# Optimization experiments

Hardware: AMD Instinct MI355X
Metric: run time of the kernel (lower is better)

The kernel has to match this reference:

```python
import jax, jax.numpy as jnp
import numpy as np

DIM = 768
DEPTH = 6
HEADS = 12
DIM_HEAD = 64
INNER = HEADS * DIM_HEAD  # 768
MLP = DIM * 4
B, N = 4, 2048
EPS = 1e-5


def setup_inputs() -> dict:
    key = jax.random.key(0)
    ks = jax.random.split(key, 8)
    s = lambda *sh: 0.02
    inp = {
        "x": jax.random.normal(ks[0], (B, N, DIM), dtype=jnp.float32),
        "ln1_g": jnp.ones((DEPTH, DIM), jnp.float32),
        "ln1_b": jnp.zeros((DEPTH, DIM), jnp.float32),
        "wqkv": jax.random.normal(ks[1], (DEPTH, DIM, 3 * INNER), jnp.float32) * 0.02,
        "wout": jax.random.normal(ks[2], (DEPTH, INNER, DIM), jnp.float32) * 0.02,
        "ln2_g": jnp.ones((DEPTH, DIM), jnp.float32),
        "ln2_b": jnp.zeros((DEPTH, DIM), jnp.float32),
        "w1": jax.random.normal(ks[3], (DEPTH, DIM, MLP), jnp.float32) * 0.02,
        "b1": jnp.zeros((DEPTH, MLP), jnp.float32),
        "w2": jax.random.normal(ks[4], (DEPTH, MLP, DIM), jnp.float32) * 0.02,
        "b2": jnp.zeros((DEPTH, DIM), jnp.float32),
        "fn_g": jnp.ones((DIM,), jnp.float32),
        "fn_b": jnp.zeros((DIM,), jnp.float32),
    }
    return inp


def layer_norm(x, g, b):
    mu = jnp.mean(x, axis=-1, keepdims=True)
    var = jnp.mean(jnp.square(x - mu), axis=-1, keepdims=True)
    return (x - mu) * jax.lax.rsqrt(var + EPS) * g + b


def attention(x, wqkv, wout):
    # x: [b, n, dim]
    qkv = x @ wqkv  # [b, n, 3*inner]
    q, k, v = jnp.split(qkv, 3, axis=-1)
    split_heads = lambda t: t.reshape(t.shape[0], t.shape[1], HEADS, DIM_HEAD).transpose(0, 2, 1, 3)
    q, k, v = split_heads(q), split_heads(k), split_heads(v)  # [b, h, n, d]
    scale = DIM_HEAD ** -0.5
    dots = jnp.einsum("bhnd,bhmd->bhnm", q, k) * scale
    attn = jax.nn.softmax(dots, axis=-1)
    out = jnp.einsum("bhnm,bhmd->bhnd", attn, v)
    out = out.transpose(0, 2, 1, 3).reshape(x.shape[0], x.shape[1], INNER)
    return out @ wout


def feed_forward(x, w1, b1, w2, b2):
    h = jax.nn.gelu(x @ w1 + b1, approximate=False)
    return h @ w2 + b2


def reference(x, ln1_g, ln1_b, wqkv, wout, ln2_g, ln2_b, w1, b1, w2, b2, fn_g, fn_b):
    for i in range(DEPTH):
        x = x + attention(layer_norm(x, ln1_g[i], ln1_b[i]), wqkv[i], wout[i])
        x = x + feed_forward(layer_norm(x, ln2_g[i], ln2_b[i]), w1[i], b1[i], w2[i], b2[i])
    return layer_norm(x, fn_g, fn_b)
```

## Files before the change

kernel.cpp:

```cpp
#include <hip/hip_runtime.h>
#include <hip/hip_bf16.h>

typedef unsigned short ushort_t;
typedef unsigned int uint_t;
typedef __bf16 bf16x8 __attribute__((ext_vector_type(8)));
typedef float floatx4 __attribute__((ext_vector_type(4)));
typedef float floatx16 __attribute__((ext_vector_type(16)));

#define DIM 768
#define DEPTH 6
#define HEADS 12
#define DH 64
#define MLP_DIM 3072
#define BATCH 4
#define SEQ 2048
#define MTOK (BATCH * SEQ)
#define QKV3 (3 * DIM)

__device__ __forceinline__ float bf2f(unsigned u) {
    return __uint_as_float((u & 0xffffu) << 16);
}
__device__ __forceinline__ ushort_t f2bf(float f) {
    unsigned x = __float_as_uint(f);
    return (ushort_t)((x + 0x7FFFu + ((x >> 16) & 1u)) >> 16);
}
__device__ __forceinline__ void load_lds16(const void* g, void* l) {
    __builtin_amdgcn_global_load_lds((const __attribute__((address_space(1))) uint_t*)g,
                                     (__attribute__((address_space(3))) uint_t*)l, 16, 0, 0);
}
__device__ __forceinline__ uint_t cvt_pk_bf16(float lo, float hi) {
    uint_t r;
    asm("v_cvt_pk_bf16_f32 %0, %1, %2" : "=v"(r) : "v"(lo), "v"(hi));
    return r;
}
__device__ __forceinline__ float exp2_raw(float x) {
#if __has_builtin(__builtin_amdgcn_exp2f)
    return __builtin_amdgcn_exp2f(x);
#else
    return exp2f(x);
#endif
}

__global__ __launch_bounds__(256) void transpose_cvt(const float* __restrict__ in,
                                                     ushort_t* __restrict__ out,
                                                     int K, int N) {
    __shared__ float tile[32][33];
    const int d = blockIdx.z;
    in += (size_t)d * K * N;
    out += (size_t)d * K * N;
    const int n0 = blockIdx.x * 32, k0 = blockIdx.y * 32;
    for (int i = threadIdx.y; i < 32; i += 8) {
        tile[i][threadIdx.x] = in[(size_t)(k0 + i) * N + n0 + threadIdx.x];
    }
    __syncthreads();
    for (int i = threadIdx.y; i < 32; i += 8) {
        out[(size_t)(n0 + i) * K + k0 + threadIdx.x] = f2bf(tile[threadIdx.x][i]);
    }
}

template <bool OUTBF>
__global__ __launch_bounds__(256) void layernorm_k(const float* __restrict__ x,
                                                   const float* __restrict__ g,
                                                   const float* __restrict__ bta,
                                                   void* __restrict__ out) {
    const int row = blockIdx.x, t = threadIdx.x;
    const float* xr = x + (size_t)row * DIM;
    float v0 = xr[t], v1 = xr[t + 256], v2 = xr[t + 512];
    float s = v0 + v1 + v2;
    float sq = v0 * v0 + v1 * v1 + v2 * v2;
#pragma unroll
    for (int off = 32; off > 0; off >>= 1) {
        s += __shfl_down(s, off, 64);
        sq += __shfl_down(sq, off, 64);
    }
    __shared__ float ss[4], ssq[4];
    const int w = t >> 6;
    if ((t & 63) == 0) { ss[w] = s; ssq[w] = sq; }
    __syncthreads();
    s = ss[0] + ss[1] + ss[2] + ss[3];
    sq = ssq[0] + ssq[1] + ssq[2] + ssq[3];
    const float mean = s * (1.0f / DIM);
    const float var = sq * (1.0f / DIM) - mean * mean;
    const float rstd = rsqrtf(var + 1e-5f);
    float y0 = (v0 - mean) * rstd * g[t] + bta[t];
    float y1 = (v1 - mean) * rstd * g[t + 256] + bta[t + 256];
    float y2 = (v2 - mean) * rstd * g[t + 512] + bta[t + 512];
    if (OUTBF) {
        ushort_t* o = (ushort_t*)out + (size_t)row * DIM;
        o[t] = f2bf(y0); o[t + 256] = f2bf(y1); o[t + 512] = f2bf(y2);
    } else {
        float* o = (float*)out + (size_t)row * DIM;
        o[t] = y0; o[t + 256] = y1; o[t + 512] = y2;
    }
}

template <bool BIAS, bool GELU, bool RES, bool OUTBF>
__global__ __launch_bounds__(512) void gemm8(const ushort_t* __restrict__ A,
                                             const ushort_t* __restrict__ Bt,
                                             const float* __restrict__ bias,
                                             const float* __restrict__ resid,
                                             void* __restrict__ Cout,
                                             int M, int N, int K) {
    __shared__ ushort_t lds[3 * 24576];
    const int t = threadIdx.x;
    const int lane = t & 63, w = t >> 6;
    const int wm = w >> 2, wn = w & 3;

    const int nwg = gridDim.x * gridDim.y;
    int bid = blockIdx.y * gridDim.x + blockIdx.x;
    bid = (bid & 7) * (nwg >> 3) + (bid >> 3);
    const int bx = bid % gridDim.x, by = bid / gridDim.x;
    const int bm = by * 128, bn = bx * 256;

    floatx4 acc[4][4];
#pragma unroll
    for (int i = 0; i < 4; i++)
#pragma unroll
        for (int j = 0; j < 4; j++) acc[i][j] = (floatx4)0.0f;

    const int srow = t >> 3;
    const int sw = ((t & 7) ^ ((t >> 3) & 7)) * 8;
    const ushort_t* Ab = A + (size_t)(bm + srow) * K + sw;
    const ushort_t* Bb = Bt + (size_t)(bn + srow) * K + sw;

    const int nk = K >> 6;
    auto stage = [&](int kt) {
        ushort_t* ls = lds + (kt % 3) * 24576;
        const int k0 = kt * 64;
        load_lds16(Ab + k0, ls + t * 8);
        load_lds16(Ab + (size_t)64 * K + k0, ls + 4096 + t * 8);
        ushort_t* lb = ls + 8192;
        load_lds16(Bb + k0, lb + t * 8);
        load_lds16(Bb + (size_t)64 * K + k0, lb + 4096 + t * 8);
        load_lds16(Bb + (size_t)128 * K + k0, lb + 8192 + t * 8);
        load_lds16(Bb + (size_t)192 * K + k0, lb + 12288 + t * 8);
    };

    stage(0);
    if (nk > 1) stage(1);

    const int l15 = lane & 15, quad = lane >> 4;
    const int arow = wm * 64 + l15;
    const int brow = wn * 64 + l15;
    const int swz = l15 & 7;

    for (int kt = 0; kt < nk; kt++) {
        if (kt < nk - 1) asm volatile("s_waitcnt vmcnt(6)" ::: "memory");
        else             asm volatile("s_waitcnt vmcnt(0)" ::: "memory");
        __builtin_amdgcn_s_barrier();
        if (kt + 2 < nk) stage(kt + 2);
        const ushort_t* Al = lds + (kt % 3) * 24576;
        const ushort_t* Bl = Al + 8192;
#pragma unroll
        for (int ks = 0; ks < 2; ks++) {
            const int kc = ((ks * 4 + quad) ^ swz) * 8;
            bf16x8 af[4], bf[4];
#pragma unroll
            for (int i = 0; i < 4; i++)
                af[i] = *(const bf16x8*)(Al + (arow + i * 16) * 64 + kc);
#pragma unroll
            for (int j = 0; j < 4; j++)
                bf[j] = *(const bf16x8*)(Bl + (brow + j * 16) * 64 + kc);
#pragma unroll
            for (int i = 0; i < 4; i++)
#pragma unroll
                for (int j = 0; j < 4; j++)
                    acc[i][j] = __builtin_amdgcn_mfma_f32_16x16x32_bf16(af[i], bf[j], acc[i][j], 0, 0, 0);
        }
    }

    const int colq = lane & 15, rq = lane >> 4;
#pragma unroll
    for (int j = 0; j < 4; j++) {
        const int col = bn + wn * 64 + j * 16 + colq;
        const float bv = BIAS ? bias[col] : 0.0f;
#pragma unroll
        for (int i = 0; i < 4; i++) {
#pragma unroll
            for (int r = 0; r < 4; r++) {
                const int row = bm + wm * 64 + i * 16 + rq * 4 + r;
                float v = acc[i][j][r] + bv;
                if (GELU) v = 0.5f * v * (1.0f + erff(v * 0.70710678118654752f));
                const size_t idx = (size_t)row * N + col;
                if (RES) v += resid[idx];
                if (OUTBF) ((ushort_t*)Cout)[idx] = f2bf(v);
                else ((float*)Cout)[idx] = v;
            }
        }
    }
}

#define TSTR 66

__global__ __launch_bounds__(256) void v_transpose(const ushort_t* __restrict__ qkv,
                                                   ushort_t* __restrict__ vt) {
    __shared__ ushort_t tile[64 * TSTR];
    const int t = threadIdx.x;
    const int tk = blockIdx.x, h = blockIdx.y, b = blockIdx.z;
#pragma unroll
    for (int rep = 0; rep < 2; rep++) {
        const int s = t + rep * 256;
        const int row = s >> 3, uo = (s & 7) * 8;
        *(uint4*)(tile + row * TSTR + uo) =
            *(const uint4*)(qkv + (size_t)(b * SEQ + tk * 64 + row) * QKV3 + 2 * DIM + h * DH + uo);
    }
    __syncthreads();
#pragma unroll
    for (int rep = 0; rep < 2; rep++) {
        const int s = t + rep * 256;
        const int d = s >> 3, to = (s & 7) * 8;
        ushort_t tmp[8];
#pragma unroll
        for (int j = 0; j < 8; j++) tmp[j] = tile[(to + j) * TSTR + d];
        *(uint4*)(vt + ((size_t)(b * HEADS + h) * DH + d) * SEQ + tk * 64 + to) = *(uint4*)tmp;
    }
}

#define SC2 0.18033688011112042f

__global__ __launch_bounds__(256, 3) void attn_mfma(const ushort_t* __restrict__ qkv,
                                                    const ushort_t* __restrict__ vt,
                                                    ushort_t* __restrict__ outp) {
    __shared__ ushort_t lds_k[2][64 * 64];
    __shared__ ushort_t lds_vt[2][64 * 64];

    const int t = threadIdx.x;
    const int lane = t & 63, w = t >> 6;
    const int h = blockIdx.y, b = blockIdx.z;
    const int q0 = blockIdx.x * 128 + w * 32;
    const int l31 = lane & 31, hi = lane >> 5;

    bf16x8 qf[4];
#pragma unroll
    for (int dc = 0; dc < 4; dc++) {
        const uint4 raw = *(const uint4*)(qkv + (size_t)(b * SEQ + q0 + l31) * QKV3 +
                                          h * DH + dc * 16 + hi * 8);
        const uint_t rr[4] = {raw.x, raw.y, raw.z, raw.w};
        union { ushort_t u[8]; bf16x8 v; } qq;
#pragma unroll
        for (int e = 0; e < 4; e++) {
            qq.u[2 * e] = f2bf(bf2f(rr[e]) * SC2);
            qq.u[2 * e + 1] = f2bf(bf2f(rr[e] >> 16) * SC2);
        }
        qf[dc] = qq.v;
    }

    union { ushort_t u[8]; bf16x8 v; } onef;
#pragma unroll
    for (int e = 0; e < 8; e++) onef.u[e] = 0x3F80;

    floatx16 o[2];
    o[0] = (floatx16)0.0f; o[1] = (floatx16)0.0f;
    floatx16 osum = (floatx16)0.0f;

    const int srow = w * 16 + (lane >> 3);
    const int sg = ((lane & 7) ^ ((lane >> 3) & 7)) * 8;
    const ushort_t* kgbase = qkv + (size_t)(b * SEQ + srow) * QKV3 + DIM + h * DH + sg;
    const ushort_t* vgbase = vt + ((size_t)(b * HEADS + h) * DH + srow) * SEQ + sg;

    auto stage = [&](int kt) {
        const int bsel = kt & 1;
        ushort_t* ldk = (ushort_t*)lds_k[bsel] + w * 16 * 64;
        ushort_t* ldv = (ushort_t*)lds_vt[bsel] + w * 16 * 64;
        const ushort_t* kg = kgbase + (size_t)kt * 64 * QKV3;
        const ushort_t* vg = vgbase + kt * 64;
        load_lds16(kg, ldk);
        load_lds16(kg + (size_t)8 * QKV3, ldk + 8 * 64);
        load_lds16(vg, ldv);
        load_lds16(vg + (size_t)8 * SEQ, ldv + 8 * 64);
    };

    stage(0);
    for (int kt = 0; kt < SEQ / 64; kt++) {
        __syncthreads();
        stage((kt + 1) & (SEQ / 64 - 1));
        const ushort_t* ldk = lds_k[kt & 1];
        const ushort_t* ldv = lds_vt[kt & 1];

#pragma unroll
        for (int kt2 = 0; kt2 < 2; kt2++) {
            const int krow = kt2 * 32 + l31;
            const int ksw = krow & 7;
            floatx16 s = (floatx16)0.0f;
#pragma unroll
            for (int dc = 0; dc < 4; dc++) {
                const bf16x8 kf = *(const bf16x8*)(ldk + krow * 64 + ((dc * 2 + hi) ^ ksw) * 8);
                s = __builtin_amdgcn_mfma_f32_32x32x16_bf16(kf, qf[dc], s, 0, 0, 0);
            }

            bf16x8 vfr[2][2];
#pragma unroll
            for (int kc = 0; kc < 2; kc++)
#pragma unroll
                for (int dhalf = 0; dhalf < 2; dhalf++) {
                    const int vrow = dhalf * 32 + l31;
                    const int kcg = kt2 * 2 + kc;
                    vfr[kc][dhalf] =
                        *(const bf16x8*)(ldv + vrow * 64 + (((kcg * 2 + hi) ^ (vrow & 7)) * 8));
                }

            float p[16];
#pragma unroll
            for (int r = 0; r < 16; r++) p[r] = exp2_raw(s[r]);

#pragma unroll
            for (int kc = 0; kc < 2; kc++) {
                uint_t da = cvt_pk_bf16(p[kc * 8 + 0], p[kc * 8 + 1]);
                uint_t db = cvt_pk_bf16(p[kc * 8 + 2], p[kc * 8 + 3]);
                uint_t dcq = cvt_pk_bf16(p[kc * 8 + 4], p[kc * 8 + 5]);
                uint_t dd = cvt_pk_bf16(p[kc * 8 + 6], p[kc * 8 + 7]);
                asm volatile("v_permlane32_swap_b32 %0, %1" : "+v"(da), "+v"(dcq));
                asm volatile("v_permlane32_swap_b32 %0, %1" : "+v"(db), "+v"(dd));
                union { uint_t u[4]; bf16x8 v; } pa;
                pa.u[0] = da; pa.u[1] = db; pa.u[2] = dcq; pa.u[3] = dd;
                osum = __builtin_amdgcn_mfma_f32_32x32x16_bf16(pa.v, onef.v, osum, 0, 0, 0);
                o[0] = __builtin_amdgcn_mfma_f32_32x32x16_bf16(pa.v, vfr[kc][0], o[0], 0, 0, 0);
                o[1] = __builtin_amdgcn_mfma_f32_32x32x16_bf16(pa.v, vfr[kc][1], o[1], 0, 0, 0);
            }
        }
    }

#pragma unroll
    for (int r = 0; r < 16; r++) {
        const int ql = (r & 3) + 8 * (r >> 2) + 4 * hi;
        const float inv = 1.0f / osum[r];
        const size_t rowbase = (size_t)(b * SEQ + q0 + ql) * DIM + h * DH;
        outp[rowbase + l31] = f2bf(o[0][r] * inv);
        outp[rowbase + 32 + l31] = f2bf(o[1][r] * inv);
    }
}

extern "C" void kernel_launch(void* const* d_in, const int* in_sizes, int n_in,
                              void* d_out, int out_size, void* d_ws, size_t ws_size,
                              hipStream_t stream) {
    const float* x_in  = (const float*)d_in[0];
    const float* ln1_g = (const float*)d_in[1];
    const float* ln1_b = (const float*)d_in[2];
    const float* wqkv  = (const float*)d_in[3];
    const float* wout  = (const float*)d_in[4];
    const float* ln2_g = (const float*)d_in[5];
    const float* ln2_b = (const float*)d_in[6];
    const float* w1    = (const float*)d_in[7];
    const float* b1    = (const float*)d_in[8];
    const float* w2    = (const float*)d_in[9];
    const float* b2    = (const float*)d_in[10];
    const float* fn_g  = (const float*)d_in[11];
    const float* fn_b  = (const float*)d_in[12];

    char* ws = (char*)d_ws;
    size_t off = 0;
    auto alloc = [&](size_t bytes) -> char* {
        char* p = ws + off;
        off = (off + bytes + 255) & ~(size_t)255;
        return p;
    };
    ushort_t* wT_qkv = (ushort_t*)alloc((size_t)DEPTH * QKV3 * DIM * 2);
    ushort_t* wT_out = (ushort_t*)alloc((size_t)DEPTH * DIM * DIM * 2);
    ushort_t* wT_1   = (ushort_t*)alloc((size_t)DEPTH * MLP_DIM * DIM * 2);
    ushort_t* wT_2   = (ushort_t*)alloc((size_t)DEPTH * DIM * MLP_DIM * 2);
    float*    xbuf   = (float*)alloc((size_t)MTOK * DIM * 4);
    ushort_t* lnbuf  = (ushort_t*)alloc((size_t)MTOK * DIM * 2);
    ushort_t* qkvbuf = (ushort_t*)alloc((size_t)MTOK * QKV3 * 2);
    ushort_t* attnbuf= (ushort_t*)alloc((size_t)MTOK * DIM * 2);
    ushort_t* hbuf   = (ushort_t*)alloc((size_t)MTOK * MLP_DIM * 2);
    ushort_t* vtbuf  = hbuf;
    (void)ws_size; (void)in_sizes; (void)n_in; (void)out_size;

    transpose_cvt<<<dim3(QKV3 / 32, DIM / 32, DEPTH), dim3(32, 8), 0, stream>>>(wqkv, wT_qkv, DIM, QKV3);
    transpose_cvt<<<dim3(DIM / 32, DIM / 32, DEPTH), dim3(32, 8), 0, stream>>>(wout, wT_out, DIM, DIM);
    transpose_cvt<<<dim3(MLP_DIM / 32, DIM / 32, DEPTH), dim3(32, 8), 0, stream>>>(w1, wT_1, DIM, MLP_DIM);
    transpose_cvt<<<dim3(DIM / 32, MLP_DIM / 32, DEPTH), dim3(32, 8), 0, stream>>>(w2, wT_2, MLP_DIM, DIM);

    hipMemcpyAsync(xbuf, x_in, (size_t)MTOK * DIM * sizeof(float), hipMemcpyDeviceToDevice, stream);

    for (int i = 0; i < DEPTH; i++) {
        layernorm_k<true><<<MTOK, 256, 0, stream>>>(xbuf, ln1_g + i * DIM, ln1_b + i * DIM, lnbuf);
        gemm8<false, false, false, true><<<dim3(QKV3 / 256, MTOK / 128), 512, 0, stream>>>(
            lnbuf, wT_qkv + (size_t)i * QKV3 * DIM, nullptr, nullptr, qkvbuf, MTOK, QKV3, DIM);
        v_transpose<<<dim3(SEQ / 64, HEADS, BATCH), 256, 0, stream>>>(qkvbuf, vtbuf);
        attn_mfma<<<dim3(SEQ / 128, HEADS, BATCH), 256, 0, stream>>>(qkvbuf, vtbuf, attnbuf);
        gemm8<false, false, true, false><<<dim3(DIM / 256, MTOK / 128), 512, 0, stream>>>(
            attnbuf, wT_out + (size_t)i * DIM * DIM, nullptr, xbuf, xbuf, MTOK, DIM, DIM);
        layernorm_k<true><<<MTOK, 256, 0, stream>>>(xbuf, ln2_g + i * DIM, ln2_b + i * DIM, lnbuf);
        gemm8<true, true, false, true><<<dim3(MLP_DIM / 256, MTOK / 128), 512, 0, stream>>>(
            lnbuf, wT_1 + (size_t)i * MLP_DIM * DIM, b1 + (size_t)i * MLP_DIM, nullptr, hbuf, MTOK, MLP_DIM, DIM);
        gemm8<true, false, true, false><<<dim3(DIM / 256, MTOK / 128), 512, 0, stream>>>(
            hbuf, wT_2 + (size_t)i * DIM * MLP_DIM, b2 + (size_t)i * DIM, xbuf, xbuf, MTOK, DIM, MLP_DIM);
    }
    layernorm_k<false><<<MTOK, 256, 0, stream>>>(xbuf, fn_g, fn_b, (float*)d_out);
}
```

Measured before the change: 1.931 ms.

## Interleave global-to-LDS prefetch with MFMA sub-steps and raise priority during MFMA

Splits the stage of the next-next tile's global-to-LDS loads across the two k sub-steps, so each sub-step issues three async loads after its LDS fragment reads. It adds extra barriers, an explicit lgkmcnt wait and a sched_barrier, and wraps the MFMA block in s_setprio to favour matrix issue. The goal is to spread memory traffic across compute in a ping-pong style schedule. The cost is extra barriers per k-step, which may stall waves, and the vmcnt(6) wait accounting still has to match the load count.

```diff
diff --git a/kernel.cpp b/kernel.cpp
--- a/kernel.cpp
+++ b/kernel.cpp
@@ -129,11 +129,10 @@
         const int k0 = kt * 64;
         load_lds16(Ab + k0, ls + t * 8);
         load_lds16(Ab + (size_t)64 * K + k0, ls + 4096 + t * 8);
-        ushort_t* lb = ls + 8192;
-        load_lds16(Bb + k0, lb + t * 8);
-        load_lds16(Bb + (size_t)64 * K + k0, lb + 4096 + t * 8);
-        load_lds16(Bb + (size_t)128 * K + k0, lb + 8192 + t * 8);
-        load_lds16(Bb + (size_t)192 * K + k0, lb + 12288 + t * 8);
+        load_lds16(Bb + k0, ls + 8192 + t * 8);
+        load_lds16(Bb + (size_t)64 * K + k0, ls + 12288 + t * 8);
+        load_lds16(Bb + (size_t)128 * K + k0, ls + 16384 + t * 8);
+        load_lds16(Bb + (size_t)192 * K + k0, ls + 20480 + t * 8);
     };
 
     stage(0);
@@ -148,24 +147,43 @@
         if (kt < nk - 1) asm volatile("s_waitcnt vmcnt(6)" ::: "memory");
         else             asm volatile("s_waitcnt vmcnt(0)" ::: "memory");
         __builtin_amdgcn_s_barrier();
-        if (kt + 2 < nk) stage(kt + 2);
         const ushort_t* Al = lds + (kt % 3) * 24576;
         const ushort_t* Bl = Al + 8192;
+        ushort_t* ls = lds + ((kt + 2) % 3) * 24576;
+        const int k0n = (kt + 2) * 64;
+        const bool doStage = (kt + 2 < nk);
 #pragma unroll
         for (int ks = 0; ks < 2; ks++) {
             const int kc = ((ks * 4 + quad) ^ swz) * 8;
-            bf16x8 af[4], bf[4];
+            bf16x8 af[4], bfr[4];
 #pragma unroll
             for (int i = 0; i < 4; i++)
                 af[i] = *(const bf16x8*)(Al + (arow + i * 16) * 64 + kc);
 #pragma unroll
             for (int j = 0; j < 4; j++)
-                bf[j] = *(const bf16x8*)(Bl + (brow + j * 16) * 64 + kc);
+                bfr[j] = *(const bf16x8*)(Bl + (brow + j * 16) * 64 + kc);
+            if (doStage) {
+                if (ks == 0) {
+                    load_lds16(Ab + k0n, ls + t * 8);
+                    load_lds16(Ab + (size_t)64 * K + k0n, ls + 4096 + t * 8);
+                    load_lds16(Bb + k0n, ls + 8192 + t * 8);
+                } else {
+                    load_lds16(Bb + (size_t)64 * K + k0n, ls + 12288 + t * 8);
+                    load_lds16(Bb + (size_t)128 * K + k0n, ls + 16384 + t * 8);
+                    load_lds16(Bb + (size_t)192 * K + k0n, ls + 20480 + t * 8);
+                }
+            }
+            __builtin_amdgcn_s_barrier();
+            asm volatile("s_waitcnt lgkmcnt(0)" ::: "memory");
+            __builtin_amdgcn_sched_barrier(0);
+            __builtin_amdgcn_s_setprio(1);
 #pragma unroll
             for (int i = 0; i < 4; i++)
 #pragma unroll
                 for (int j = 0; j < 4; j++)
-                    acc[i][j] = __builtin_amdgcn_mfma_f32_16x16x32_bf16(af[i], bf[j], acc[i][j], 0, 0, 0);
+                    acc[i][j] = __builtin_amdgcn_mfma_f32_16x16x32_bf16(af[i], bfr[j], acc[i][j], 0, 0, 0);
+            __builtin_amdgcn_s_setprio(0);
+            if (ks == 0) __builtin_amdgcn_s_barrier();
         }
     }
 
```

Measured after the change: 1.934 ms. About the same (+0.2%).

## Use 256x256 tiled GEMM for QKV and FFN1, fast erf-based GELU

Applied to the files above, without the earlier changes.

Adds a gemm256 kernel with 256x256 output tiles, double-buffered LDS staging, and 8x4 MFMA accumulators per wave, used for the QKV projection and the first MLP layer. The larger tiles raise arithmetic intensity and cut global traffic per FLOP. The cost is higher register pressure and fewer workgroups: QKV drops to 288 blocks, which may under-fill the GPU. It also replaces erff in GELU with an Abramowitz-Stegun polynomial approximation using a fast reciprocal and exp2, which lowers epilogue cost at slightly reduced accuracy.

```diff
diff --git a/kernel.cpp b/kernel.cpp
--- a/kernel.cpp
+++ b/kernel.cpp
@@ -39,6 +39,27 @@
 #else
     return exp2f(x);
 #endif
+}
+__device__ __forceinline__ float rcp_fast(float x) {
+#if __has_builtin(__builtin_amdgcn_rcpf)
+    return __builtin_amdgcn_rcpf(x);
+#else
+    return 1.0f / x;
+#endif
+}
+__device__ __forceinline__ float gelu_fast(float v) {
+    const float z = v * 0.70710678118654752f;
+    const float az = fabsf(z);
+    const float tt = rcp_fast(fmaf(0.3275911f, az, 1.0f));
+    const float e = exp2_raw(-1.44269504088896f * az * az);
+    float p = fmaf(1.061405429f, tt, -1.453152027f);
+    p = fmaf(p, tt, 1.421413741f);
+    p = fmaf(p, tt, -0.284496736f);
+    p = fmaf(p, tt, 0.254829592f);
+    p = p * tt;
+    float erfz = fmaf(-p, e, 1.0f);
+    erfz = copysignf(erfz, z);
+    return 0.5f * v * (1.0f + erfz);
 }
 
 __global__ __launch_bounds__(256) void transpose_cvt(const float* __restrict__ in,
@@ -94,6 +115,91 @@
     }
 }
 
+template <bool BIAS, bool GELU>
+__global__ __launch_bounds__(512) void gemm256(const ushort_t* __restrict__ A,
+                                               const ushort_t* __restrict__ Bt,
+                                               const float* __restrict__ bias,
+                                               ushort_t* __restrict__ Cout,
+                                               int M, int N, int K) {
+    __shared__ ushort_t lds[2][32768];
+    const int t = threadIdx.x;
+    const int lane = t & 63, w = t >> 6;
+    const int wm = w >> 2, wn = w & 3;
+
+    const int nwg = gridDim.x * gridDim.y;
+    int bid = blockIdx.y * gridDim.x + blockIdx.x;
+    bid = (bid & 7) * (nwg >> 3) + (bid >> 3);
+    const int bx = bid % gridDim.x, by = bid / gridDim.x;
+    const int bm = by * 256, bn = bx * 256;
+
+    floatx4 acc[8][4];
+#pragma unroll
+    for (int i = 0; i < 8; i++)
+#pragma unroll
+        for (int j = 0; j < 4; j++) acc[i][j] = (floatx4)0.0f;
+
+    const int srow = t >> 3;
+    const int sw = ((t & 7) ^ ((t >> 3) & 7)) * 8;
+    const ushort_t* Ab = A + (size_t)(bm + srow) * K + sw;
+    const ushort_t* Bb = Bt + (size_t)(bn + srow) * K + sw;
+
+    const int nk = K >> 6;
+    auto stage = [&](int kt) {
+        ushort_t* ls = lds[kt & 1];
+        const int k0 = kt * 64;
+#pragma unroll
+        for (int r2 = 0; r2 < 4; r2++) {
+            load_lds16(Ab + (size_t)(64 * r2) * K + k0, ls + r2 * 4096 + t * 8);
+            load_lds16(Bb + (size_t)(64 * r2) * K + k0, ls + 16384 + r2 * 4096 + t * 8);
+        }
+    };
+
+    stage(0);
+    const int l15 = lane & 15, quad = lane >> 4;
+    const int arow = wm * 128 + l15;
+    const int brow = wn * 64 + l15;
+    const int swz = l15 & 7;
+
+    for (int kt = 0; kt < nk; kt++) {
+        __syncthreads();
+        if (kt + 1 < nk) stage(kt + 1);
+        const ushort_t* Al = lds[kt & 1];
+        const ushort_t* Bl = Al + 16384;
+#pragma unroll
+        for (int ks = 0; ks < 2; ks++) {
+            const int kc = ((ks * 4 + quad) ^ swz) * 8;
+            bf16x8 bfr[4];
+#pragma unroll
+            for (int j = 0; j < 4; j++)
+                bfr[j] = *(const bf16x8*)(Bl + (brow + j * 16) * 64 + kc);
+#pragma unroll
+            for (int i = 0; i < 8; i++) {
+                const bf16x8 af = *(const bf16x8*)(Al + (arow + i * 16) * 64 + kc);
+#pragma unroll
+                for (int j = 0; j < 4; j++)
+                    acc[i][j] = __builtin_amdgcn_mfma_f32_16x16x32_bf16(af, bfr[j], acc[i][j], 0, 0, 0);
+            }
+        }
+    }
+
+    const int colq = lane & 15, rq = lane >> 4;
+#pragma unroll
+    for (int j = 0; j < 4; j++) {
+        const int col = bn + wn * 64 + j * 16 + colq;
+        const float bv = BIAS ? bias[col] : 0.0f;
+#pragma unroll
+        for (int i = 0; i < 8; i++) {
+#pragma unroll
+            for (int r = 0; r < 4; r++) {
+                const int row = bm + wm * 128 + i * 16 + rq * 4 + r;
+                float v = acc[i][j][r] + bv;
+                if (GELU) v = gelu_fast(v);
+                Cout[(size_t)row * N + col] = f2bf(v);
+            }
+        }
+    }
+}
+
 template <bool BIAS, bool GELU, bool RES, bool OUTBF>
 __global__ __launch_bounds__(512) void gemm8(const ushort_t* __restrict__ A,
                                              const ushort_t* __restrict__ Bt,
@@ -154,20 +260,21 @@
 #pragma unroll
         for (int ks = 0; ks < 2; ks++) {
             const int kc = ((ks * 4 + quad) ^ swz) * 8;
-            bf16x8 af[4], bf[4];
+            bf16x8 af[4], bfr[4];
 #pragma unroll
             for (int i = 0; i < 4; i++)
                 af[i] = *(const bf16x8*)(Al + (arow + i * 16) * 64 + kc);
 #pragma unroll
             for (int j = 0; j < 4; j++)
-                bf[j] = *(const bf16x8*)(Bl + (brow + j * 16) * 64 + kc);
+                bfr[j] = *(const bf16x8*)(Bl + (brow + j * 16) * 64 + kc);
 #pragma unroll
             for (int i = 0; i < 4; i++)
 #pragma unroll
                 for (int j = 0; j < 4; j++)
-                    acc[i][j] = __builtin_amdgcn_mfma_f32_16x16x32_bf16(af[i], bf[j], acc[i][j], 0, 0, 0);
-        }
-    }
+                    acc[i][j] = __builtin_amdgcn_mfma_f32_16x16x32_bf16(af[i], bfr[j], acc[i][j], 0, 0, 0);
+        }
+    }
+    asm volatile("s_waitcnt vmcnt(0)" ::: "memory");
 
     const int colq = lane & 15, rq = lane >> 4;
 #pragma unroll
@@ -180,7 +287,7 @@
             for (int r = 0; r < 4; r++) {
                 const int row = bm + wm * 64 + i * 16 + rq * 4 + r;
                 float v = acc[i][j][r] + bv;
-                if (GELU) v = 0.5f * v * (1.0f + erff(v * 0.70710678118654752f));
+                if (GELU) v = gelu_fast(v);
                 const size_t idx = (size_t)row * N + col;
                 if (RES) v += resid[idx];
                 if (OUTBF) ((ushort_t*)Cout)[idx] = f2bf(v);
@@ -375,15 +482,15 @@
 
     for (int i = 0; i < DEPTH; i++) {
         layernorm_k<true><<<MTOK, 256, 0, stream>>>(xbuf, ln1_g + i * DIM, ln1_b + i * DIM, lnbuf);
-        gemm8<false, false, false, true><<<dim3(QKV3 / 256, MTOK / 128), 512, 0, stream>>>(
-            lnbuf, wT_qkv + (size_t)i * QKV3 * DIM, nullptr, nullptr, qkvbuf, MTOK, QKV3, DIM);
+        gemm256<false, false><<<dim3(QKV3 / 256, MTOK / 256), 512, 0, stream>>>(
+            lnbuf, wT_qkv + (size_t)i * QKV3 * DIM, nullptr, qkvbuf, MTOK, QKV3, DIM);
         v_transpose<<<dim3(SEQ / 64, HEADS, BATCH), 256, 0, stream>>>(qkvbuf, vtbuf);
         attn_mfma<<<dim3(SEQ / 128, HEADS, BATCH), 256, 0, stream>>>(qkvbuf, vtbuf, attnbuf);
         gemm8<false, false, true, false><<<dim3(DIM / 256, MTOK / 128), 512, 0, stream>>>(
             attnbuf, wT_out + (size_t)i * DIM * DIM, nullptr, xbuf, xbuf, MTOK, DIM, DIM);
         layernorm_k<true><<<MTOK, 256, 0, stream>>>(xbuf, ln2_g + i * DIM, ln2_b + i * DIM, lnbuf);
-        gemm8<true, true, false, true><<<dim3(MLP_DIM / 256, MTOK / 128), 512, 0, stream>>>(
-            lnbuf, wT_1 + (size_t)i * MLP_DIM * DIM, b1 + (size_t)i * MLP_DIM, nullptr, hbuf, MTOK, MLP_DIM, DIM);
+        gemm256<true, true><<<dim3(MLP_DIM / 256, MTOK / 256), 512, 0, stream>>>(
+            lnbuf, wT_1 + (size_t)i * MLP_DIM * DIM, b1 + (size_t)i * MLP_DIM, hbuf, MTOK, MLP_DIM, DIM);
         gemm8<true, false, true, false><<<dim3(DIM / 256, MTOK / 128), 512, 0, stream>>>(
             hbuf, wT_2 + (size_t)i * DIM * MLP_DIM, b2 + (size_t)i * DIM, xbuf, xbuf, MTOK, DIM, MLP_DIM);
     }
```

After: 1.895 ms. No clear change (-1.8%).
